# Optimization experiments

Hardware: AMD Instinct MI355X
Metric: run time of the kernel (lower is better)

The kernel has to match this reference:

```python
import jax, jax.numpy as jnp
import numpy as np

B, S, H = 1, 2048, 2048
NH, NKV, HD = 32, 8, 64
GROUPS = NH // NKV
ROPE_BASE = 10000.0
NEG = -1e9


def setup_inputs() -> dict:
    key = jax.random.key(0)
    ks = jax.random.split(key, 5)
    hidden_states = jax.random.normal(ks[0], (B, S, H), dtype=jnp.float32)
    # causal additive mask: 0 on/below diagonal, large negative above
    causal = jnp.tril(jnp.ones((S, S), dtype=bool))
    attention_mask = jnp.where(causal, 0.0, NEG).astype(jnp.float32)[None, None]
    position_ids = jnp.arange(S, dtype=jnp.int64)[None, :].astype(jnp.int32)
    sc = 1.0 / np.sqrt(H)
    Wq = jax.random.normal(ks[1], (NH * HD, H), dtype=jnp.float32) * sc
    Wk = jax.random.normal(ks[2], (NKV * HD, H), dtype=jnp.float32) * sc
    Wv = jax.random.normal(ks[3], (NKV * HD, H), dtype=jnp.float32) * sc
    Wo = jax.random.normal(ks[4], (H, H), dtype=jnp.float32) * sc
    return {"hidden_states": hidden_states, "attention_mask": attention_mask,
            "position_ids": position_ids, "Wq": Wq, "Wk": Wk, "Wv": Wv, "Wo": Wo}


def _rotate_half(x):
    x1, x2 = jnp.split(x, 2, axis=-1)
    return jnp.concatenate((-x2, x1), axis=-1)


def _rope_cos_sin(position_ids, dtype):
    inv_freq = 1.0 / (ROPE_BASE ** (jnp.arange(0, HD, 2, dtype=jnp.float32) / HD))
    # [b, s, hd/2]
    freqs = position_ids.astype(jnp.float32)[:, :, None] * inv_freq[None, None, :]
    emb = jnp.concatenate((freqs, freqs), axis=-1)  # [b, s, hd]
    # unsqueeze head dim -> [b, 1, s, hd]
    return jnp.cos(emb).astype(dtype)[:, None], jnp.sin(emb).astype(dtype)[:, None]


def reference(hidden_states, attention_mask, position_ids, Wq, Wk, Wv, Wo):
    b, s, _ = hidden_states.shape
    q = (hidden_states @ Wq.T).reshape(b, s, NH, HD).transpose(0, 2, 1, 3)
    k = (hidden_states @ Wk.T).reshape(b, s, NKV, HD).transpose(0, 2, 1, 3)
    v = (hidden_states @ Wv.T).reshape(b, s, NKV, HD).transpose(0, 2, 1, 3)

    cos, sin = _rope_cos_sin(position_ids, hidden_states.dtype)
    q = q * cos + _rotate_half(q) * sin
    k = k * cos + _rotate_half(k) * sin

    # GQA: duplicate KV heads (repeat_interleave along head dim)
    k = jnp.repeat(k, GROUPS, axis=1)
    v = jnp.repeat(v, GROUPS, axis=1)

    scale = 1.0 / jnp.sqrt(jnp.asarray(HD, dtype=hidden_states.dtype))
    scores = jnp.einsum('bhqd,bhkd->bhqk', q, k) * scale + attention_mask
    attn = jax.nn.softmax(scores, axis=-1)
    out = jnp.einsum('bhqk,bhkd->bhqd', attn, v)
    out = out.transpose(0, 2, 1, 3).reshape(b, s, NH * HD)
    return out @ Wo.T
```

## Files before the change

### kernel.cpp

```cpp
#include <hip/hip_runtime.h>
#include <math.h>

#define S_LEN 2048
#define HID   2048
#define NH    32
#define NKV   8
#define HD    64
#define BK    32

typedef short short4x __attribute__((ext_vector_type(4)));
typedef short short8  __attribute__((ext_vector_type(8)));
typedef float floatx4 __attribute__((ext_vector_type(4)));

static __device__ __forceinline__ ushort f2bf(float f) {
  unsigned u = __float_as_uint(f);
  u += 0x7fffu + ((u >> 16) & 1u);
  return (ushort)(u >> 16);
}

static __device__ __forceinline__ void gl2lds16(const ushort* g, ushort* l) {
  __builtin_amdgcn_global_load_lds(
      (const __attribute__((address_space(1))) unsigned int*)g,
      (__attribute__((address_space(3))) unsigned int*)l, 16, 0, 0);
}

__global__ void cvt_bf16_kernel(const float* __restrict__ src,
                                ushort* __restrict__ dst, int n4) {
  int i = blockIdx.x * 256 + threadIdx.x;
  if (i >= n4) return;
  float4 v = ((const float4*)src)[i];
  ushort4 o;
  o.x = f2bf(v.x); o.y = f2bf(v.y); o.z = f2bf(v.z); o.w = f2bf(v.w);
  ((ushort4*)dst)[i] = o;
}

__global__ __launch_bounds__(256) void gemm128_bt_kernel(
    const ushort* __restrict__ A, const ushort* __restrict__ B,
    float* __restrict__ C, int M, int N, int K) {
  __shared__ __align__(16) ushort As[128 * BK];
  __shared__ __align__(16) ushort Bs[128 * BK];

  const int tid  = threadIdx.x;
  const int wave = tid >> 6;
  const int lane = tid & 63;
  const int r16  = lane & 15;
  const int quad = lane >> 4;

  const int m_base = blockIdx.y * 128;
  const int n_base = blockIdx.x * 128;
  const int wm = (wave & 1) * 64;
  const int wn = (wave >> 1) * 64;

  const int srow = wave * 32 + (lane >> 2);
  const int scol = (lane & 3) * 8;
  const ushort* ag0 = A + (size_t)(m_base + srow) * K + scol;
  const ushort* ag1 = ag0 + (size_t)16 * K;
  const ushort* bg0 = B + (size_t)(n_base + srow) * K + scol;
  const ushort* bg1 = bg0 + (size_t)16 * K;
  ushort* as0 = As + (wave * 32) * BK;
  ushort* as1 = As + (wave * 32 + 16) * BK;
  ushort* bs0 = Bs + (wave * 32) * BK;
  ushort* bs1 = Bs + (wave * 32 + 16) * BK;

  floatx4 acc[4][4];
#pragma unroll
  for (int i = 0; i < 4; ++i)
#pragma unroll
    for (int j = 0; j < 4; ++j) acc[i][j] = floatx4{0.f, 0.f, 0.f, 0.f};

  for (int kk = 0; kk < K; kk += BK) {
    __syncthreads();
    gl2lds16(ag0 + kk, as0);
    gl2lds16(ag1 + kk, as1);
    gl2lds16(bg0 + kk, bs0);
    gl2lds16(bg1 + kk, bs1);
    __syncthreads();

    short8 af[4], bf[4];
#pragma unroll
    for (int i = 0; i < 4; ++i)
      af[i] = *(const short8*)&As[(wm + i * 16 + r16) * BK + quad * 8];
#pragma unroll
    for (int j = 0; j < 4; ++j)
      bf[j] = *(const short8*)&Bs[(wn + j * 16 + r16) * BK + quad * 8];
#pragma unroll
    for (int i = 0; i < 4; ++i)
#pragma unroll
      for (int j = 0; j < 4; ++j)
        acc[i][j] = __builtin_amdgcn_mfma_f32_16x16x32_bf16(af[i], bf[j], acc[i][j], 0, 0, 0);
  }

#pragma unroll
  for (int i = 0; i < 4; ++i)
#pragma unroll
    for (int j = 0; j < 4; ++j) {
      const int cm = m_base + wm + i * 16 + quad * 4;
      const int cn = n_base + wn + j * 16 + r16;
#pragma unroll
      for (int r = 0; r < 4; ++r)
        C[(size_t)(cm + r) * N + cn] = acc[i][j][r];
    }
}

__global__ void rope_kernel(const float* __restrict__ lin,
                            ushort* __restrict__ outp,
                            const int* __restrict__ pos_ids,
                            int nh, int sh, int ld) {
  int idx = blockIdx.x * 256 + threadIdx.x;
  int d2 = idx & 31;
  int h  = (idx >> 5) & (nh - 1);
  int s  = idx >> (5 + sh);
  float pos  = (float)pos_ids[s];
  float invf = powf(10000.0f, -(2.0f * (float)d2) * (1.0f / 64.0f));
  float sn, cs;
  sincosf(pos * invf, &sn, &cs);
  float x1 = lin[(size_t)s * ld + h * 64 + d2];
  float x2 = lin[(size_t)s * ld + h * 64 + d2 + 32];
  outp[((size_t)h * S_LEN + s) * 64 + d2]      = f2bf(x1 * cs - x2 * sn);
  outp[((size_t)h * S_LEN + s) * 64 + d2 + 32] = f2bf(x2 * cs + x1 * sn);
}

__global__ void transpose_v_kernel(const float* __restrict__ lin,
                                   ushort* __restrict__ vt, int ld) {
  int idx = blockIdx.x * 256 + threadIdx.x;
  int s4 = idx & (S_LEN / 4 - 1);
  int d  = (idx >> 9) & 63;
  int h  = idx >> 15;
  const float* src = lin + (size_t)(s4 * 4) * ld + h * 64 + d;
  ushort4 o;
  o.x = f2bf(src[0 * ld]);
  o.y = f2bf(src[1 * ld]);
  o.z = f2bf(src[2 * ld]);
  o.w = f2bf(src[3 * ld]);
  ((ushort4*)vt)[idx] = o;
}

#define LOG2E_SC 0.180336880f

__global__ __launch_bounds__(256) void attn_kernel(
    const ushort* __restrict__ Q,
    const ushort* __restrict__ K,
    const ushort* __restrict__ Vt,
    ushort* __restrict__ O) {
  __shared__ __align__(16) ushort Ks[64][72];
  __shared__ __align__(16) ushort Vs[64][72];
  __shared__ __align__(16) ushort Pw[4][16][72];

  const int h    = blockIdx.x;
  const int kh   = h >> 2;
  const int y    = blockIdx.y;
  const int qt   = (y & 1) ? (31 - (y >> 1)) : (y >> 1);
  const int tid  = threadIdx.x;
  const int wave = tid >> 6;
  const int lane = tid & 63;
  const int r16  = lane & 15;
  const int quad = lane >> 4;

  const ushort* qp = Q + ((size_t)h * S_LEN + qt * 64 + wave * 16 + r16) * 64 + quad * 8;
  const short8 qf0 = *(const short8*)(qp);
  const short8 qf1 = *(const short8*)(qp + 32);

  const int q_glob = qt * 64 + wave * 16 + r16;

  float m_run = -1e30f, l_run = 0.f;
  floatx4 oacc[4];
#pragma unroll
  for (int n = 0; n < 4; ++n) oacc[n] = floatx4{0.f, 0.f, 0.f, 0.f};

  for (int kt = 0; kt <= qt; ++kt) {
    __syncthreads();
    {
      const ushort* ksrc = K  + ((size_t)kh * S_LEN + kt * 64) * 64;
      const ushort* vsrc = Vt + ((size_t)kh * 64) * S_LEN + kt * 64;
#pragma unroll
      for (int i = tid; i < 512; i += 256) {
        int r = i >> 3, c = (i & 7) * 8;
        *(short8*)&Ks[r][c] = *(const short8*)(ksrc + (size_t)r * 64 + c);
        *(short8*)&Vs[r][c] = *(const short8*)(vsrc + (size_t)r * S_LEN + c);
      }
    }
    __syncthreads();

    floatx4 sacc[4];
#pragma unroll
    for (int t = 0; t < 4; ++t) {
      short8 kf0 = *(const short8*)&Ks[t * 16 + r16][quad * 8];
      short8 kf1 = *(const short8*)&Ks[t * 16 + r16][32 + quad * 8];
      floatx4 z = {0.f, 0.f, 0.f, 0.f};
      z = __builtin_amdgcn_mfma_f32_16x16x32_bf16(kf0, qf0, z, 0, 0, 0);
      sacc[t] = __builtin_amdgcn_mfma_f32_16x16x32_bf16(kf1, qf1, z, 0, 0, 0);
    }

    const bool diag = (kt == qt);
#pragma unroll
    for (int t = 0; t < 4; ++t)
#pragma unroll
      for (int r = 0; r < 4; ++r) {
        float sc = sacc[t][r] * LOG2E_SC;
        if (diag && (kt * 64 + t * 16 + quad * 4 + r) > q_glob) sc = -1e30f;
        sacc[t][r] = sc;
      }

    float mx = -1e30f;
#pragma unroll
    for (int t = 0; t < 4; ++t)
#pragma unroll
      for (int r = 0; r < 4; ++r) mx = fmaxf(mx, sacc[t][r]);
    mx = fmaxf(mx, __shfl_xor(mx, 16));
    mx = fmaxf(mx, __shfl_xor(mx, 32));
    float mnew  = fmaxf(m_run, mx);
    float alpha = __builtin_amdgcn_exp2f(m_run - mnew);
    m_run = mnew;

    float ps = 0.f;
#pragma unroll
    for (int t = 0; t < 4; ++t) {
      float p0 = __builtin_amdgcn_exp2f(sacc[t][0] - mnew);
      float p1 = __builtin_amdgcn_exp2f(sacc[t][1] - mnew);
      float p2 = __builtin_amdgcn_exp2f(sacc[t][2] - mnew);
      float p3 = __builtin_amdgcn_exp2f(sacc[t][3] - mnew);
      ps += (p0 + p1) + (p2 + p3);
      *(short4x*)&Pw[wave][r16][t * 16 + quad * 4] =
          short4x{(short)f2bf(p0), (short)f2bf(p1),
                  (short)f2bf(p2), (short)f2bf(p3)};
    }
    ps += __shfl_xor(ps, 16);
    ps += __shfl_xor(ps, 32);
    l_run = l_run * alpha + ps;

    short8 pf0 = *(const short8*)&Pw[wave][r16][quad * 8];
    short8 pf1 = *(const short8*)&Pw[wave][r16][32 + quad * 8];
#pragma unroll
    for (int n = 0; n < 4; ++n) {
      oacc[n][0] *= alpha; oacc[n][1] *= alpha;
      oacc[n][2] *= alpha; oacc[n][3] *= alpha;
      short8 vf0 = *(const short8*)&Vs[n * 16 + r16][quad * 8];
      short8 vf1 = *(const short8*)&Vs[n * 16 + r16][32 + quad * 8];
      oacc[n] = __builtin_amdgcn_mfma_f32_16x16x32_bf16(vf0, pf0, oacc[n], 0, 0, 0);
      oacc[n] = __builtin_amdgcn_mfma_f32_16x16x32_bf16(vf1, pf1, oacc[n], 0, 0, 0);
    }
  }

  const float inv_l = 1.f / l_run;
#pragma unroll
  for (int n = 0; n < 4; ++n) {
    ushort4 o4;
    o4.x = f2bf(oacc[n][0] * inv_l);
    o4.y = f2bf(oacc[n][1] * inv_l);
    o4.z = f2bf(oacc[n][2] * inv_l);
    o4.w = f2bf(oacc[n][3] * inv_l);
    *(ushort4*)&O[(size_t)q_glob * (NH * HD) + h * 64 + n * 16 + quad * 4] = o4;
  }
}

extern "C" void kernel_launch(void* const* d_in, const int* in_sizes, int n_in,
                              void* d_out, int out_size, void* d_ws, size_t ws_size,
                              hipStream_t stream) {
  const float* hidden = (const float*)d_in[0];
  const int*   pos    = (const int*)d_in[2];
  const float* Wq     = (const float*)d_in[3];
  const float* Wk     = (const float*)d_in[4];
  const float* Wv     = (const float*)d_in[5];
  const float* Wo     = (const float*)d_in[6];
  float* out = (float*)d_out;

  const int NQKV = HID + 2 * NKV * HD;

  char* w = (char*)d_ws;
  auto carve = [&](size_t bytes) { char* p = w; w += bytes; return p; };
  ushort* hb    = (ushort*)carve((size_t)S_LEN * HID * 2);
  ushort* wqkvb = (ushort*)carve((size_t)NQKV * HID * 2);
  ushort* wob   = (ushort*)carve((size_t)HID * HID * 2);
  float*  qkvl  = (float*)carve((size_t)S_LEN * NQKV * 4);
  ushort* qr    = (ushort*)carve((size_t)NH * S_LEN * HD * 2);
  ushort* kr    = (ushort*)carve((size_t)NKV * S_LEN * HD * 2);
  ushort* vtb   = (ushort*)carve((size_t)NKV * HD * S_LEN * 2);
  ushort* ob    = (ushort*)carve((size_t)S_LEN * HID * 2);

  cvt_bf16_kernel<<<(S_LEN * HID / 4) / 256, 256, 0, stream>>>(hidden, hb, S_LEN * HID / 4);
  cvt_bf16_kernel<<<(HID * HID / 4) / 256, 256, 0, stream>>>(Wq, wqkvb, HID * HID / 4);
  cvt_bf16_kernel<<<(NKV * HD * HID / 4) / 256, 256, 0, stream>>>(
      Wk, wqkvb + (size_t)HID * HID, NKV * HD * HID / 4);
  cvt_bf16_kernel<<<(NKV * HD * HID / 4) / 256, 256, 0, stream>>>(
      Wv, wqkvb + (size_t)(HID + NKV * HD) * HID, NKV * HD * HID / 4);
  cvt_bf16_kernel<<<(HID * HID / 4) / 256, 256, 0, stream>>>(Wo, wob, HID * HID / 4);

  dim3 gqkv(NQKV / 128, S_LEN / 128);
  gemm128_bt_kernel<<<gqkv, 256, 0, stream>>>(hb, wqkvb, qkvl, S_LEN, NQKV, HID);

  rope_kernel<<<(S_LEN * NH * 32) / 256, 256, 0, stream>>>(qkvl, qr, pos, NH, 5, NQKV);
  rope_kernel<<<(S_LEN * NKV * 32) / 256, 256, 0, stream>>>(qkvl + HID, kr, pos, NKV, 3, NQKV);
  transpose_v_kernel<<<(NKV * HD * S_LEN / 4) / 256, 256, 0, stream>>>(
      qkvl + HID + NKV * HD, vtb, NQKV);

  dim3 ga(NH, S_LEN / 64);
  attn_kernel<<<ga, 256, 0, stream>>>(qr, kr, vtb, ob);

  dim3 go(HID / 128, S_LEN / 128);
  gemm128_bt_kernel<<<go, 256, 0, stream>>>(ob, wob, out, S_LEN, HID, HID);
}
```

Measured before the change: 302.4 us.

## Fuse RoPE and V transpose into QKV GEMM epilogue, merge bf16 conversions

```diff
diff --git a/kernel.cpp b/kernel.cpp
--- a/kernel.cpp
+++ b/kernel.cpp
@@ -24,14 +24,30 @@
       (__attribute__((address_space(3))) unsigned int*)l, 16, 0, 0);
 }
 
-__global__ void cvt_bf16_kernel(const float* __restrict__ src,
-                                ushort* __restrict__ dst, int n4) {
-  int i = blockIdx.x * 256 + threadIdx.x;
-  if (i >= n4) return;
-  float4 v = ((const float4*)src)[i];
+#define QH  1048576
+#define QW  1048576
+#define QKq  262144
+#define QVq  262144
+#define QO  1048576
+__global__ void cvt_all_kernel(const float* __restrict__ h,
+                               const float* __restrict__ wq,
+                               const float* __restrict__ wk,
+                               const float* __restrict__ wv,
+                               const float* __restrict__ wo,
+                               ushort* __restrict__ hb,
+                               ushort* __restrict__ wqkvb,
+                               ushort* __restrict__ wob) {
+  int idx = blockIdx.x * 256 + threadIdx.x;
+  const float* src; ushort* dst; int so, dqo;
+  if (idx < QH)                    { src = h;  dst = hb;    so = idx;                   dqo = so; }
+  else if (idx < QH + QW)          { src = wq; dst = wqkvb; so = idx - QH;              dqo = so; }
+  else if (idx < QH + QW + QKq)    { src = wk; dst = wqkvb; so = idx - QH - QW;         dqo = so + QW; }
+  else if (idx < QH + QW + QKq + QVq) { src = wv; dst = wqkvb; so = idx - QH - QW - QKq; dqo = so + QW + QKq; }
+  else                             { src = wo; dst = wob;   so = idx - QH - QW - QKq - QVq; dqo = so; }
+  float4 v = ((const float4*)src)[so];
   ushort4 o;
   o.x = f2bf(v.x); o.y = f2bf(v.y); o.z = f2bf(v.z); o.w = f2bf(v.w);
-  ((ushort4*)dst)[i] = o;
+  ((ushort4*)dst)[dqo] = o;
 }
 
 __global__ __launch_bounds__(256) void gemm128_bt_kernel(
@@ -102,37 +118,106 @@
     }
 }
 
-__global__ void rope_kernel(const float* __restrict__ lin,
-                            ushort* __restrict__ outp,
-                            const int* __restrict__ pos_ids,
-                            int nh, int sh, int ld) {
-  int idx = blockIdx.x * 256 + threadIdx.x;
-  int d2 = idx & 31;
-  int h  = (idx >> 5) & (nh - 1);
-  int s  = idx >> (5 + sh);
-  float pos  = (float)pos_ids[s];
-  float invf = powf(10000.0f, -(2.0f * (float)d2) * (1.0f / 64.0f));
-  float sn, cs;
-  sincosf(pos * invf, &sn, &cs);
-  float x1 = lin[(size_t)s * ld + h * 64 + d2];
-  float x2 = lin[(size_t)s * ld + h * 64 + d2 + 32];
-  outp[((size_t)h * S_LEN + s) * 64 + d2]      = f2bf(x1 * cs - x2 * sn);
-  outp[((size_t)h * S_LEN + s) * 64 + d2 + 32] = f2bf(x2 * cs + x1 * sn);
-}
-
-__global__ void transpose_v_kernel(const float* __restrict__ lin,
-                                   ushort* __restrict__ vt, int ld) {
-  int idx = blockIdx.x * 256 + threadIdx.x;
-  int s4 = idx & (S_LEN / 4 - 1);
-  int d  = (idx >> 9) & 63;
-  int h  = idx >> 15;
-  const float* src = lin + (size_t)(s4 * 4) * ld + h * 64 + d;
-  ushort4 o;
-  o.x = f2bf(src[0 * ld]);
-  o.y = f2bf(src[1 * ld]);
-  o.z = f2bf(src[2 * ld]);
-  o.w = f2bf(src[3 * ld]);
-  ((ushort4*)vt)[idx] = o;
+__global__ __launch_bounds__(256) void gemm_qkv_kernel(
+    const ushort* __restrict__ A, const ushort* __restrict__ B,
+    const int* __restrict__ pos,
+    ushort* __restrict__ qr,
+    ushort* __restrict__ kr,
+    ushort* __restrict__ vtb) {
+  __shared__ __align__(16) ushort As[128 * BK];
+  __shared__ __align__(16) ushort Bs[128 * BK];
+
+  const int K = HID;
+  const int tid  = threadIdx.x;
+  const int wave = tid >> 6;
+  const int lane = tid & 63;
+  const int r16  = lane & 15;
+  const int quad = lane >> 4;
+
+  const int m_base = blockIdx.y * 128;
+  const int n_base = blockIdx.x * 128;
+  const int wm = (wave & 1) * 64;
+  const int wn = (wave >> 1) * 64;
+
+  const int srow = wave * 32 + (lane >> 2);
+  const int scol = (lane & 3) * 8;
+  const ushort* ag0 = A + (size_t)(m_base + srow) * K + scol;
+  const ushort* ag1 = ag0 + (size_t)16 * K;
+  const ushort* bg0 = B + (size_t)(n_base + srow) * K + scol;
+  const ushort* bg1 = bg0 + (size_t)16 * K;
+  ushort* as0 = As + (wave * 32) * BK;
+  ushort* as1 = As + (wave * 32 + 16) * BK;
+  ushort* bs0 = Bs + (wave * 32) * BK;
+  ushort* bs1 = Bs + (wave * 32 + 16) * BK;
+
+  floatx4 acc[4][4];
+#pragma unroll
+  for (int i = 0; i < 4; ++i)
+#pragma unroll
+    for (int j = 0; j < 4; ++j) acc[i][j] = floatx4{0.f, 0.f, 0.f, 0.f};
+
+  for (int kk = 0; kk < K; kk += BK) {
+    __syncthreads();
+    gl2lds16(ag0 + kk, as0);
+    gl2lds16(ag1 + kk, as1);
+    gl2lds16(bg0 + kk, bs0);
+    gl2lds16(bg1 + kk, bs1);
+    __syncthreads();
+
+    short8 af[4], bf[4];
+#pragma unroll
+    for (int i = 0; i < 4; ++i)
+      af[i] = *(const short8*)&As[(wm + i * 16 + r16) * BK + quad * 8];
+#pragma unroll
+    for (int j = 0; j < 4; ++j)
+      bf[j] = *(const short8*)&Bs[(wn + j * 16 + r16) * BK + quad * 8];
+#pragma unroll
+    for (int i = 0; i < 4; ++i)
+#pragma unroll
+      for (int j = 0; j < 4; ++j)
+        acc[i][j] = __builtin_amdgcn_mfma_f32_16x16x32_bf16(af[i], bf[j], acc[i][j], 0, 0, 0);
+  }
+
+  const int n0w = n_base + wn;
+  if (n0w < HID + NKV * HD) {
+    ushort* dst;
+    if (n0w < HID) dst = qr + (size_t)(n0w >> 6) * S_LEN * 64;
+    else           dst = kr + (size_t)((n0w - HID) >> 6) * S_LEN * 64;
+    const float invfA = powf(10000.0f, -(float)r16 * (1.0f / 32.0f));
+    const float invfB = powf(10000.0f, -(float)(16 + r16) * (1.0f / 32.0f));
+#pragma unroll
+    for (int i = 0; i < 4; ++i) {
+#pragma unroll
+      for (int r = 0; r < 4; ++r) {
+        const int s = m_base + wm + i * 16 + quad * 4 + r;
+        const float p = (float)pos[s];
+        float snA, csA, snB, csB;
+        sincosf(p * invfA, &snA, &csA);
+        sincosf(p * invfB, &snB, &csB);
+        ushort* row = dst + (size_t)s * 64;
+        row[r16]      = f2bf(acc[i][0][r] * csA - acc[i][2][r] * snA);
+        row[16 + r16] = f2bf(acc[i][1][r] * csB - acc[i][3][r] * snB);
+        row[32 + r16] = f2bf(acc[i][2][r] * csA + acc[i][0][r] * snA);
+        row[48 + r16] = f2bf(acc[i][3][r] * csB + acc[i][1][r] * snB);
+      }
+    }
+  } else {
+    const int hh = (n0w - HID - NKV * HD) >> 6;
+#pragma unroll
+    for (int i = 0; i < 4; ++i) {
+      const int s0 = m_base + wm + i * 16 + quad * 4;
+#pragma unroll
+      for (int j = 0; j < 4; ++j) {
+        const int d = j * 16 + r16;
+        ushort4 o4;
+        o4.x = f2bf(acc[i][j][0]);
+        o4.y = f2bf(acc[i][j][1]);
+        o4.z = f2bf(acc[i][j][2]);
+        o4.w = f2bf(acc[i][j][3]);
+        *(ushort4*)&vtb[((size_t)hh * 64 + d) * S_LEN + s0] = o4;
+      }
+    }
+  }
 }
 
 #define LOG2E_SC 0.180336880f
@@ -271,27 +356,16 @@
   ushort* hb    = (ushort*)carve((size_t)S_LEN * HID * 2);
   ushort* wqkvb = (ushort*)carve((size_t)NQKV * HID * 2);
   ushort* wob   = (ushort*)carve((size_t)HID * HID * 2);
-  float*  qkvl  = (float*)carve((size_t)S_LEN * NQKV * 4);
   ushort* qr    = (ushort*)carve((size_t)NH * S_LEN * HD * 2);
   ushort* kr    = (ushort*)carve((size_t)NKV * S_LEN * HD * 2);
   ushort* vtb   = (ushort*)carve((size_t)NKV * HD * S_LEN * 2);
   ushort* ob    = (ushort*)carve((size_t)S_LEN * HID * 2);
 
-  cvt_bf16_kernel<<<(S_LEN * HID / 4) / 256, 256, 0, stream>>>(hidden, hb, S_LEN * HID / 4);
-  cvt_bf16_kernel<<<(HID * HID / 4) / 256, 256, 0, stream>>>(Wq, wqkvb, HID * HID / 4);
-  cvt_bf16_kernel<<<(NKV * HD * HID / 4) / 256, 256, 0, stream>>>(
-      Wk, wqkvb + (size_t)HID * HID, NKV * HD * HID / 4);
-  cvt_bf16_kernel<<<(NKV * HD * HID / 4) / 256, 256, 0, stream>>>(
-      Wv, wqkvb + (size_t)(HID + NKV * HD) * HID, NKV * HD * HID / 4);
-  cvt_bf16_kernel<<<(HID * HID / 4) / 256, 256, 0, stream>>>(Wo, wob, HID * HID / 4);
+  cvt_all_kernel<<<(QH + QW + QKq + QVq + QO) / 256, 256, 0, stream>>>(
+      hidden, Wq, Wk, Wv, Wo, hb, wqkvb, wob);
 
   dim3 gqkv(NQKV / 128, S_LEN / 128);
-  gemm128_bt_kernel<<<gqkv, 256, 0, stream>>>(hb, wqkvb, qkvl, S_LEN, NQKV, HID);
-
-  rope_kernel<<<(S_LEN * NH * 32) / 256, 256, 0, stream>>>(qkvl, qr, pos, NH, 5, NQKV);
-  rope_kernel<<<(S_LEN * NKV * 32) / 256, 256, 0, stream>>>(qkvl + HID, kr, pos, NKV, 3, NQKV);
-  transpose_v_kernel<<<(NKV * HD * S_LEN / 4) / 256, 256, 0, stream>>>(
-      qkvl + HID + NKV * HD, vtb, NQKV);
+  gemm_qkv_kernel<<<gqkv, 256, 0, stream>>>(hb, wqkvb, pos, qr, kr, vtb);
 
   dim3 ga(NH, S_LEN / 64);
   attn_kernel<<<ga, 256, 0, stream>>>(qr, kr, vtb, ob);
```

New measurement: 267.7 us. 11.5% less time.
